# Performance work log

Measured on AMD Instinct MI355X. Metric: run time of the kernel, lower is better.

## Reference

```python
import jax, jax.numpy as jnp
import numpy as np

MESSAGE_PASSES = 3
HID = 100        # hidden_node_features == message_size
EDGE_F = 4       # n_edge_features
OUT = 100        # readout output dim


def setup_inputs() -> dict:
    key = jax.random.key(0)
    ks = jax.random.split(key, 8)
    B, N = 32, 128
    nodes = jax.random.normal(ks[0], (B, N, HID), dtype=jnp.float32)
    edges = jax.random.uniform(ks[1], (B, N, N, EDGE_F), dtype=jnp.float32)
    s = 1.0 / np.sqrt(HID)
    Wv = jax.random.normal(ks[2], (HID, HID), dtype=jnp.float32) * s
    Ww = jax.random.normal(ks[3], (HID, HID), dtype=jnp.float32) * s
    We = jax.random.normal(ks[4], (EDGE_F, HID), dtype=jnp.float32) * (1.0 / np.sqrt(EDGE_F))
    Wu = jax.random.normal(ks[5], (2 * HID, HID), dtype=jnp.float32) * (1.0 / np.sqrt(2 * HID))
    Wr = jax.random.normal(ks[6], (2 * HID, OUT), dtype=jnp.float32) * (1.0 / np.sqrt(2 * HID))
    return {"nodes": nodes, "edges": edges, "Wv": Wv, "Ww": Ww, "We": We, "Wu": Wu, "Wr": Wr}


def reference(nodes, edges, Wv, Ww, We, Wu, Wr):
    # adjacency[b,v,w] = sum_e edges[b,v,w,e]; nonzero entries define the edge set
    adjacency = edges.sum(axis=-1)                       # [B,N,N]
    edge_mask = adjacency != 0                           # [B,N,N]
    node_mask = adjacency.sum(axis=-1) != 0              # [B,N]

    # edge feature projection is constant across message passes
    e_proj = jnp.einsum('bvwe,eh->bvwh', edges, We)      # [B,N,N,H]

    hidden = nodes                                       # hidden_node_features == node feat dim
    for _ in range(MESSAGE_PASSES):
        # message_terms for every (b, v, w) edge: relu(h_v Wv + h_w Ww + e_vw We)
        pre = (hidden @ Wv)[:, :, None, :] + (hidden @ Ww)[:, None, :, :] + e_proj
        mterms = jnp.where(edge_mask[..., None], jax.nn.relu(pre), 0.0)
        # (same_batch * same_node) matmul == segment-sum over neighbors w
        messages = mterms.sum(axis=2)                    # [B,N,H]
        # update only nodes that appear in the edge set (degree > 0)
        upd = jnp.tanh(jnp.concatenate([hidden, messages], axis=-1) @ Wu)
        hidden = jnp.where(node_mask[..., None], upd, hidden)

    # readout: masked sum-pool of per-node graph terms
    graph_terms = jax.nn.relu(jnp.concatenate([hidden, nodes], axis=-1) @ Wr)  # [B,N,OUT]
    output = jnp.where(node_mask[..., None], graph_terms, 0.0).sum(axis=1)     # [B,OUT]
    return output
```

## Files before the change

### kernel.cpp

```cpp
#include <hip/hip_runtime.h>
#include <math.h>

#define B_   32
#define N_   128
#define H_   100
#define ROWS (B_ * N_)
#define RH   (ROWS * H_)

__global__ __launch_bounds__(256) void k_mask(const float* __restrict__ edges,
                                              float* __restrict__ nmask) {
    const int t = threadIdx.x, lane = t & 63, wv = t >> 6;
    const int row = blockIdx.x * 4 + wv;
    const float4* eg = (const float4*)(edges + (size_t)row * N_ * 4);
    const float4 e0 = eg[lane], e1 = eg[lane + 64];
    const float s0 = (e0.x + e0.y) + (e0.z + e0.w);
    const float s1 = (e1.x + e1.y) + (e1.z + e1.w);
    const unsigned long long bl = __ballot((s0 != 0.f) || (s1 != 0.f));
    if (lane == 0) nmask[row] = bl ? 1.f : 0.f;
}

__global__ __launch_bounds__(256, 6) void k_proj0(const float* __restrict__ nodes,
                                                  const float* __restrict__ Wv,
                                                  const float* __restrict__ Ww,
                                                  float* __restrict__ hv,
                                                  float* __restrict__ hw) {
    __shared__ float nod_s[2][H_];
    const int row0 = blockIdx.x * 2;
    const int t = threadIdx.x, r = t >> 7, j = t & 127;
    {
        const float4* ng = (const float4*)(nodes + (size_t)row0 * H_);
        if (t < 50) ((float4*)nod_s)[t] = ng[t];
    }
    __syncthreads();
    if (j >= H_) return;
    const float* hr = nod_s[r];
    float va = 0.f, wa = 0.f;
#pragma unroll 4
    for (int k = 0; k < H_; ++k) {
        const float hk = hr[k];
        va = fmaf(hk, Wv[k * H_ + j], va);
        wa = fmaf(hk, Ww[k * H_ + j], wa);
    }
    hv[(size_t)(row0 + r) * H_ + j] = va;
    hw[(size_t)(row0 + r) * H_ + j] = wa;
}

__global__ __launch_bounds__(256, 6) void k_pass(const float* __restrict__ edges,
                                                 const float* __restrict__ We,
                                                 const float* __restrict__ Wu,
                                                 const float* __restrict__ Wv,
                                                 const float* __restrict__ Ww,
                                                 const float* __restrict__ nmask,
                                                 float* __restrict__ hv_io,
                                                 const float* __restrict__ hw_in,
                                                 float* __restrict__ hw_out,
                                                 const float* __restrict__ hid_in,
                                                 float* __restrict__ hidden,
                                                 int do_proj) {
    __shared__ float4 e_s[2][N_];
    __shared__ float  m_s[2][N_];
    __shared__ float  hid_s[2][H_];
    __shared__ float  msg_s[2][H_];
    __shared__ float  hn_s[2][H_];

    const int row0 = blockIdx.x * 2;
    const int b = row0 >> 7;
    const int t = threadIdx.x, r = t >> 7, j = t & 127;
    const int row = row0 + r;

    {
        const float4* eg = (const float4*)(edges + (size_t)row0 * N_ * 4);
        const float4 e = eg[t];
        e_s[r][j] = e;
        const float s = (e.x + e.y) + (e.z + e.w);
        m_s[r][j] = (s != 0.f) ? 1.f : 0.f;
    }
    {
        const float4* hg = (const float4*)(hid_in + (size_t)row0 * H_);
        if (t < 50) ((float4*)hid_s)[t] = hg[t];
    }
    __syncthreads();

    const bool act = (j < H_);
    if (act) {
        const float hvv = hv_io[(size_t)row * H_ + j];
        const float we0 = We[0 * H_ + j], we1 = We[1 * H_ + j];
        const float we2 = We[2 * H_ + j], we3 = We[3 * H_ + j];
        const float* hwp = hw_in + (size_t)b * N_ * H_ + j;
        float acc = 0.f;
#pragma unroll 8
        for (int w = 0; w < N_; ++w) {
            const float  hww = hwp[w * H_];
            const float4 e = e_s[r][w];
            const float  m = m_s[r][w];
            float p = hvv + hww;
            p = fmaf(e.x, we0, p);
            p = fmaf(e.y, we1, p);
            p = fmaf(e.z, we2, p);
            p = fmaf(e.w, we3, p);
            acc = fmaf(m, fmaxf(p, 0.f), acc);
        }
        msg_s[r][j] = acc;
    }
    __syncthreads();

    float nh = 0.f;
    if (act) {
        const float* hr = hid_s[r];
        const float* mr = msg_s[r];
        float u = 0.f;
#pragma unroll 8
        for (int k = 0; k < H_; ++k)
            u = fmaf(hr[k], Wu[k * H_ + j], u);
#pragma unroll 8
        for (int k = 0; k < H_; ++k)
            u = fmaf(mr[k], Wu[(H_ + k) * H_ + j], u);
        const float nm = nmask[row];
        nh = (nm != 0.f) ? tanhf(u) : hr[j];
        hidden[(size_t)row * H_ + j] = nh;
        if (do_proj) hn_s[r][j] = nh;
    }

    if (do_proj) {
        __syncthreads();
        if (act) {
            const float* hr = hn_s[r];
            float va = 0.f, wa = 0.f;
#pragma unroll 4
            for (int k = 0; k < H_; ++k) {
                const float hk = hr[k];
                va = fmaf(hk, Wv[k * H_ + j], va);
                wa = fmaf(hk, Ww[k * H_ + j], wa);
            }
            hv_io[(size_t)row * H_ + j] = va;
            hw_out[(size_t)row * H_ + j] = wa;
        }
    }
}

__global__ __launch_bounds__(256, 6) void k_readout(const float* __restrict__ hidden,
                                                    const float* __restrict__ nodes,
                                                    const float* __restrict__ Wr,
                                                    const float* __restrict__ nmask,
                                                    float* __restrict__ out) {
    __shared__ float hid_s[2][H_], nod_s[2][H_], red_s[2][H_];
    const int row0 = blockIdx.x * 2, b = row0 >> 7;
    const int t = threadIdx.x, r = t >> 7, j = t & 127;
    const int row = row0 + r;
    {
        const float4* hg = (const float4*)(hidden + (size_t)row0 * H_);
        const float4* ng = (const float4*)(nodes + (size_t)row0 * H_);
        if (t < 50) {
            ((float4*)hid_s)[t] = hg[t];
            ((float4*)nod_s)[t] = ng[t];
        }
    }
    __syncthreads();
    if (j < H_) {
        const float* hr = hid_s[r];
        const float* nr = nod_s[r];
        float u = 0.f;
#pragma unroll 8
        for (int k = 0; k < H_; ++k)
            u = fmaf(hr[k], Wr[k * H_ + j], u);
#pragma unroll 8
        for (int k = 0; k < H_; ++k)
            u = fmaf(nr[k], Wr[(H_ + k) * H_ + j], u);
        red_s[r][j] = nmask[row] * fmaxf(u, 0.f);
    }
    __syncthreads();
    if (t < H_) atomicAdd(out + b * H_ + t, red_s[0][t] + red_s[1][t]);
}

extern "C" void kernel_launch(void* const* d_in, const int* in_sizes, int n_in,
                              void* d_out, int out_size, void* d_ws, size_t ws_size,
                              hipStream_t stream) {
    const float* nodes = (const float*)d_in[0];
    const float* edges = (const float*)d_in[1];
    const float* Wv    = (const float*)d_in[2];
    const float* Ww    = (const float*)d_in[3];
    const float* We    = (const float*)d_in[4];
    const float* Wu    = (const float*)d_in[5];
    const float* Wr    = (const float*)d_in[6];
    float* out = (float*)d_out;

    float* hidden = (float*)d_ws;
    float* hv     = hidden + RH;
    float* hwA    = hv + RH;
    float* hwB    = hwA + RH;
    float* nmask  = hwB + RH;

    hipMemsetAsync(d_out, 0, (size_t)out_size * sizeof(float), stream);

    k_mask<<<ROWS / 4, 256, 0, stream>>>(edges, nmask);
    k_proj0<<<ROWS / 2, 256, 0, stream>>>(nodes, Wv, Ww, hv, hwA);

    k_pass<<<ROWS / 2, 256, 0, stream>>>(edges, We, Wu, Wv, Ww, nmask,
                                         hv, hwA, hwB, nodes, hidden, 1);
    k_pass<<<ROWS / 2, 256, 0, stream>>>(edges, We, Wu, Wv, Ww, nmask,
                                         hv, hwB, hwA, hidden, hidden, 1);
    k_pass<<<ROWS / 2, 256, 0, stream>>>(edges, We, Wu, Wv, Ww, nmask,
                                         hv, hwA, hwB, hidden, hidden, 0);

    k_readout<<<ROWS / 2, 256, 0, stream>>>(hidden, nodes, Wr, nmask, out);
}
```

Before: 212.3 us.

## Fuse mask and readout into message pass kernel, vectorize smem reads

Drops the separate mask kernel and computes the node mask inside the message loop from the edge row sum. The readout is folded into the last pass, so that kernel no longer writes hidden to global memory and two launches go away. Edges are now read straight from global memory per thread instead of being staged through shared memory. Shared-memory reads in the matvecs now load float4 values. Each active thread reads the whole edge row itself, so the same edge data is read many more times through the cache.

```diff
diff --git a/kernel.cpp b/kernel.cpp
--- a/kernel.cpp
+++ b/kernel.cpp
@@ -6,18 +6,6 @@
 #define H_   100
 #define ROWS (B_ * N_)
 #define RH   (ROWS * H_)
-
-__global__ __launch_bounds__(256) void k_mask(const float* __restrict__ edges,
-                                              float* __restrict__ nmask) {
-    const int t = threadIdx.x, lane = t & 63, wv = t >> 6;
-    const int row = blockIdx.x * 4 + wv;
-    const float4* eg = (const float4*)(edges + (size_t)row * N_ * 4);
-    const float4 e0 = eg[lane], e1 = eg[lane + 64];
-    const float s0 = (e0.x + e0.y) + (e0.z + e0.w);
-    const float s1 = (e1.x + e1.y) + (e1.z + e1.w);
-    const unsigned long long bl = __ballot((s0 != 0.f) || (s1 != 0.f));
-    if (lane == 0) nmask[row] = bl ? 1.f : 0.f;
-}
 
 __global__ __launch_bounds__(256, 6) void k_proj0(const float* __restrict__ nodes,
                                                   const float* __restrict__ Wv,
@@ -33,13 +21,20 @@
     }
     __syncthreads();
     if (j >= H_) return;
-    const float* hr = nod_s[r];
+    const float4* hr4 = (const float4*)nod_s[r];
     float va = 0.f, wa = 0.f;
-#pragma unroll 4
-    for (int k = 0; k < H_; ++k) {
-        const float hk = hr[k];
-        va = fmaf(hk, Wv[k * H_ + j], va);
-        wa = fmaf(hk, Ww[k * H_ + j], wa);
+#pragma unroll 5
+    for (int k4 = 0; k4 < 25; ++k4) {
+        const float4 h4 = hr4[k4];
+        const int k = k4 * 4;
+        va = fmaf(h4.x, Wv[(k + 0) * H_ + j], va);
+        wa = fmaf(h4.x, Ww[(k + 0) * H_ + j], wa);
+        va = fmaf(h4.y, Wv[(k + 1) * H_ + j], va);
+        wa = fmaf(h4.y, Ww[(k + 1) * H_ + j], wa);
+        va = fmaf(h4.z, Wv[(k + 2) * H_ + j], va);
+        wa = fmaf(h4.z, Ww[(k + 2) * H_ + j], wa);
+        va = fmaf(h4.w, Wv[(k + 3) * H_ + j], va);
+        wa = fmaf(h4.w, Ww[(k + 3) * H_ + j], wa);
     }
     hv[(size_t)(row0 + r) * H_ + j] = va;
     hw[(size_t)(row0 + r) * H_ + j] = wa;
@@ -50,49 +45,52 @@
                                                  const float* __restrict__ Wu,
                                                  const float* __restrict__ Wv,
                                                  const float* __restrict__ Ww,
-                                                 const float* __restrict__ nmask,
+                                                 const float* __restrict__ Wr,
+                                                 const float* __restrict__ nodes,
                                                  float* __restrict__ hv_io,
                                                  const float* __restrict__ hw_in,
                                                  float* __restrict__ hw_out,
                                                  const float* __restrict__ hid_in,
                                                  float* __restrict__ hidden,
-                                                 int do_proj) {
-    __shared__ float4 e_s[2][N_];
-    __shared__ float  m_s[2][N_];
-    __shared__ float  hid_s[2][H_];
-    __shared__ float  msg_s[2][H_];
-    __shared__ float  hn_s[2][H_];
+                                                 float* __restrict__ out,
+                                                 int mode) {
+    __shared__ float hid_s[2][H_];
+    __shared__ float msg_s[2][H_];
+    __shared__ float hn_s[2][H_];
+    __shared__ float nod_s[2][H_];
+    __shared__ float red_s[2][H_];
 
     const int row0 = blockIdx.x * 2;
     const int b = row0 >> 7;
     const int t = threadIdx.x, r = t >> 7, j = t & 127;
     const int row = row0 + r;
-
-    {
-        const float4* eg = (const float4*)(edges + (size_t)row0 * N_ * 4);
-        const float4 e = eg[t];
-        e_s[r][j] = e;
-        const float s = (e.x + e.y) + (e.z + e.w);
-        m_s[r][j] = (s != 0.f) ? 1.f : 0.f;
-    }
+    const bool act = (j < H_);
+
     {
         const float4* hg = (const float4*)(hid_in + (size_t)row0 * H_);
         if (t < 50) ((float4*)hid_s)[t] = hg[t];
+        if (mode == 2) {
+            const float4* ng = (const float4*)(nodes + (size_t)row0 * H_);
+            if (t < 50) ((float4*)nod_s)[t] = ng[t];
+        }
     }
     __syncthreads();
 
-    const bool act = (j < H_);
+    float asum = 0.f;
     if (act) {
         const float hvv = hv_io[(size_t)row * H_ + j];
         const float we0 = We[0 * H_ + j], we1 = We[1 * H_ + j];
         const float we2 = We[2 * H_ + j], we3 = We[3 * H_ + j];
+        const float4* ev = (const float4*)edges + (size_t)row * N_;
         const float* hwp = hw_in + (size_t)b * N_ * H_ + j;
         float acc = 0.f;
 #pragma unroll 8
         for (int w = 0; w < N_; ++w) {
+            const float4 e = ev[w];
             const float  hww = hwp[w * H_];
-            const float4 e = e_s[r][w];
-            const float  m = m_s[r][w];
+            const float  s = (e.x + e.y) + (e.z + e.w);
+            const float  m = (s != 0.f) ? 1.f : 0.f;
+            asum += s;
             float p = hvv + hww;
             p = fmaf(e.x, we0, p);
             p = fmaf(e.y, we1, p);
@@ -104,72 +102,84 @@
     }
     __syncthreads();
 
-    float nh = 0.f;
+    const float nm = (asum != 0.f) ? 1.f : 0.f;
     if (act) {
-        const float* hr = hid_s[r];
-        const float* mr = msg_s[r];
+        const float4* hr4 = (const float4*)hid_s[r];
+        const float4* mr4 = (const float4*)msg_s[r];
         float u = 0.f;
-#pragma unroll 8
-        for (int k = 0; k < H_; ++k)
-            u = fmaf(hr[k], Wu[k * H_ + j], u);
-#pragma unroll 8
-        for (int k = 0; k < H_; ++k)
-            u = fmaf(mr[k], Wu[(H_ + k) * H_ + j], u);
-        const float nm = nmask[row];
-        nh = (nm != 0.f) ? tanhf(u) : hr[j];
-        hidden[(size_t)row * H_ + j] = nh;
-        if (do_proj) hn_s[r][j] = nh;
-    }
-
-    if (do_proj) {
+#pragma unroll 4
+        for (int k4 = 0; k4 < 25; ++k4) {
+            const float4 h4 = hr4[k4];
+            const int k = k4 * 4;
+            u = fmaf(h4.x, Wu[(k + 0) * H_ + j], u);
+            u = fmaf(h4.y, Wu[(k + 1) * H_ + j], u);
+            u = fmaf(h4.z, Wu[(k + 2) * H_ + j], u);
+            u = fmaf(h4.w, Wu[(k + 3) * H_ + j], u);
+        }
+#pragma unroll 4
+        for (int k4 = 0; k4 < 25; ++k4) {
+            const float4 m4 = mr4[k4];
+            const int k = H_ + k4 * 4;
+            u = fmaf(m4.x, Wu[(k + 0) * H_ + j], u);
+            u = fmaf(m4.y, Wu[(k + 1) * H_ + j], u);
+            u = fmaf(m4.z, Wu[(k + 2) * H_ + j], u);
+            u = fmaf(m4.w, Wu[(k + 3) * H_ + j], u);
+        }
+        const float nh = (nm != 0.f) ? tanhf(u) : hid_s[r][j];
+        hn_s[r][j] = nh;
+        if (mode == 1) hidden[(size_t)row * H_ + j] = nh;
+    }
+
+    if (mode == 1) {
         __syncthreads();
         if (act) {
-            const float* hr = hn_s[r];
+            const float4* hr4 = (const float4*)hn_s[r];
             float va = 0.f, wa = 0.f;
-#pragma unroll 4
-            for (int k = 0; k < H_; ++k) {
-                const float hk = hr[k];
-                va = fmaf(hk, Wv[k * H_ + j], va);
-                wa = fmaf(hk, Ww[k * H_ + j], wa);
+#pragma unroll 5
+            for (int k4 = 0; k4 < 25; ++k4) {
+                const float4 h4 = hr4[k4];
+                const int k = k4 * 4;
+                va = fmaf(h4.x, Wv[(k + 0) * H_ + j], va);
+                wa = fmaf(h4.x, Ww[(k + 0) * H_ + j], wa);
+                va = fmaf(h4.y, Wv[(k + 1) * H_ + j], va);
+                wa = fmaf(h4.y, Ww[(k + 1) * H_ + j], wa);
+                va = fmaf(h4.z, Wv[(k + 2) * H_ + j], va);
+                wa = fmaf(h4.z, Ww[(k + 2) * H_ + j], wa);
+                va = fmaf(h4.w, Wv[(k + 3) * H_ + j], va);
+                wa = fmaf(h4.w, Ww[(k + 3) * H_ + j], wa);
             }
             hv_io[(size_t)row * H_ + j] = va;
             hw_out[(size_t)row * H_ + j] = wa;
         }
-    }
-}
-
-__global__ __launch_bounds__(256, 6) void k_readout(const float* __restrict__ hidden,
-                                                    const float* __restrict__ nodes,
-                                                    const float* __restrict__ Wr,
-                                                    const float* __restrict__ nmask,
-                                                    float* __restrict__ out) {
-    __shared__ float hid_s[2][H_], nod_s[2][H_], red_s[2][H_];
-    const int row0 = blockIdx.x * 2, b = row0 >> 7;
-    const int t = threadIdx.x, r = t >> 7, j = t & 127;
-    const int row = row0 + r;
-    {
-        const float4* hg = (const float4*)(hidden + (size_t)row0 * H_);
-        const float4* ng = (const float4*)(nodes + (size_t)row0 * H_);
-        if (t < 50) {
-            ((float4*)hid_s)[t] = hg[t];
-            ((float4*)nod_s)[t] = ng[t];
-        }
-    }
-    __syncthreads();
-    if (j < H_) {
-        const float* hr = hid_s[r];
-        const float* nr = nod_s[r];
-        float u = 0.f;
-#pragma unroll 8
-        for (int k = 0; k < H_; ++k)
-            u = fmaf(hr[k], Wr[k * H_ + j], u);
-#pragma unroll 8
-        for (int k = 0; k < H_; ++k)
-            u = fmaf(nr[k], Wr[(H_ + k) * H_ + j], u);
-        red_s[r][j] = nmask[row] * fmaxf(u, 0.f);
-    }
-    __syncthreads();
-    if (t < H_) atomicAdd(out + b * H_ + t, red_s[0][t] + red_s[1][t]);
+    } else {
+        __syncthreads();
+        if (act) {
+            const float4* hr4 = (const float4*)hn_s[r];
+            const float4* nr4 = (const float4*)nod_s[r];
+            float u = 0.f;
+#pragma unroll 4
+            for (int k4 = 0; k4 < 25; ++k4) {
+                const float4 h4 = hr4[k4];
+                const int k = k4 * 4;
+                u = fmaf(h4.x, Wr[(k + 0) * H_ + j], u);
+                u = fmaf(h4.y, Wr[(k + 1) * H_ + j], u);
+                u = fmaf(h4.z, Wr[(k + 2) * H_ + j], u);
+                u = fmaf(h4.w, Wr[(k + 3) * H_ + j], u);
+            }
+#pragma unroll 4
+            for (int k4 = 0; k4 < 25; ++k4) {
+                const float4 n4 = nr4[k4];
+                const int k = H_ + k4 * 4;
+                u = fmaf(n4.x, Wr[(k + 0) * H_ + j], u);
+                u = fmaf(n4.y, Wr[(k + 1) * H_ + j], u);
+                u = fmaf(n4.z, Wr[(k + 2) * H_ + j], u);
+                u = fmaf(n4.w, Wr[(k + 3) * H_ + j], u);
+            }
+            red_s[r][j] = nm * fmaxf(u, 0.f);
+        }
+        __syncthreads();
+        if (t < H_) atomicAdd(out + b * H_ + t, red_s[0][t] + red_s[1][t]);
+    }
 }
 
 extern "C" void kernel_launch(void* const* d_in, const int* in_sizes, int n_in,
@@ -188,19 +198,15 @@
     float* hv     = hidden + RH;
     float* hwA    = hv + RH;
     float* hwB    = hwA + RH;
-    float* nmask  = hwB + RH;
 
     hipMemsetAsync(d_out, 0, (size_t)out_size * sizeof(float), stream);
 
-    k_mask<<<ROWS / 4, 256, 0, stream>>>(edges, nmask);
     k_proj0<<<ROWS / 2, 256, 0, stream>>>(nodes, Wv, Ww, hv, hwA);
 
-    k_pass<<<ROWS / 2, 256, 0, stream>>>(edges, We, Wu, Wv, Ww, nmask,
-                                         hv, hwA, hwB, nodes, hidden, 1);
-    k_pass<<<ROWS / 2, 256, 0, stream>>>(edges, We, Wu, Wv, Ww, nmask,
-                                         hv, hwB, hwA, hidden, hidden, 1);
-    k_pass<<<ROWS / 2, 256, 0, stream>>>(edges, We, Wu, Wv, Ww, nmask,
-                                         hv, hwA, hwB, hidden, hidden, 0);
-
-    k_readout<<<ROWS / 2, 256, 0, stream>>>(hidden, nodes, Wr, nmask, out);
+    k_pass<<<ROWS / 2, 256, 0, stream>>>(edges, We, Wu, Wv, Ww, Wr, nodes,
+                                         hv, hwA, hwB, nodes, hidden, out, 1);
+    k_pass<<<ROWS / 2, 256, 0, stream>>>(edges, We, Wu, Wv, Ww, Wr, nodes,
+                                         hv, hwB, hwA, hidden, hidden, out, 1);
+    k_pass<<<ROWS / 2, 256, 0, stream>>>(edges, We, Wu, Wv, Ww, Wr, nodes,
+                                         hv, hwA, hwB, hidden, hidden, out, 2);
 }
```

New measurement: 281.4 us. 1.33x slower.
